# Optimization experiments

Hardware: AMD Instinct MI355X
Metric: run time of the kernel (lower is better)

Reference implementation:

```python
import jax, jax.numpy as jnp
import numpy as np

B, LQ, LK, DQ, DKEY, DV = 8, 2048, 2048, 1024, 1024, 1024
MASK_NEG = -1e6  # d2l masked_softmax fill value


def setup_inputs() -> dict:
    key = jax.random.key(0)
    kq, kk, kv, kl, kw = jax.random.split(key, 5)
    queries = jax.random.normal(kq, (B, LQ, DQ), dtype=jnp.float32)
    keys = jax.random.normal(kk, (B, LK, DKEY), dtype=jnp.float32)
    values = jax.random.normal(kv, (B, LK, DV), dtype=jnp.float32)
    valid_lens = jax.random.randint(kl, (B,), 1, LK + 1)
    W_q = jax.random.normal(kw, (DQ, DKEY), dtype=jnp.float32) / np.sqrt(DQ)
    return {"queries": queries, "keys": keys, "values": values,
            "valid_lens": valid_lens, "W_q": W_q}


def reference(queries, keys, values, valid_lens, W_q):
    # Q projection: LazyLinear(key_dim, bias=False)
    q = jnp.einsum("bqd,dk->bqk", queries, W_q)          # [B, LQ, DKEY]
    d = q.shape[-1]
    scores = jnp.einsum("bqk,bsk->bqs", q, keys) / jnp.sqrt(jnp.asarray(d, q.dtype))
    # masked_softmax: positions >= valid_len set to -1e6 before softmax
    mask = jnp.arange(scores.shape[-1])[None, None, :] < valid_lens[:, None, None]
    scores = jnp.where(mask, scores, MASK_NEG)
    attn = jax.nn.softmax(scores, axis=-1)               # [B, LQ, LK]
    # dropout p=0.0 (eval) -> identity
    return jnp.einsum("bqs,bsv->bqv", attn, values)      # [B, LQ, DV]
```

## Files before the change

kernel.cpp:

```cpp
#include <hip/hip_runtime.h>
#include <cstdint>
#include <cstddef>

#define B_   8
#define LQ_  2048
#define LK_  2048

typedef __attribute__((ext_vector_type(8))) __bf16 bf16x8;
typedef __attribute__((ext_vector_type(4))) float f32x4;
typedef __attribute__((ext_vector_type(8))) unsigned short ushortx8;

__device__ __forceinline__ unsigned short f2bf(float f) {
  unsigned u = __builtin_bit_cast(unsigned, f);
  u = u + 0x7fffu + ((u >> 16) & 1u);
  return (unsigned short)(u >> 16);
}
__device__ __forceinline__ float bf2f(unsigned short h) {
  unsigned u = ((unsigned)h) << 16;
  return __builtin_bit_cast(float, u);
}

__device__ __forceinline__ void gld_lds16(const void* g, void* l) {
  __builtin_amdgcn_global_load_lds((__attribute__((address_space(1))) void*)(void*)g,
                                   (__attribute__((address_space(3))) void*)l, 16, 0, 0);
}

__global__ __launch_bounds__(256) void cast2_bf16_kernel(
    const float* __restrict__ in0, unsigned short* __restrict__ out0,
    const float* __restrict__ in1, unsigned short* __restrict__ out1,
    size_t half_blocks) {
  const float* in = blockIdx.x < half_blocks ? in0 : in1;
  unsigned short* out = blockIdx.x < half_blocks ? out0 : out1;
  size_t bb = blockIdx.x < half_blocks ? blockIdx.x : blockIdx.x - half_blocks;
  size_t i = (bb * 256 + threadIdx.x) * 8;
  float4 a = *(const float4*)(in + i);
  float4 b = *(const float4*)(in + i + 4);
  ushortx8 o;
  o[0] = f2bf(a.x); o[1] = f2bf(a.y); o[2] = f2bf(a.z); o[3] = f2bf(a.w);
  o[4] = f2bf(b.x); o[5] = f2bf(b.y); o[6] = f2bf(b.z); o[7] = f2bf(b.w);
  *(ushortx8*)(out + i) = o;
}

__global__ __launch_bounds__(256) void transpose_cast_kernel(
    const float* __restrict__ in, unsigned short* __restrict__ out,
    int R, int C, long in_bstride, long out_bstride) {
  __shared__ float t[32][33];
  const float* inb = in + (size_t)blockIdx.z * in_bstride;
  unsigned short* outb = out + (size_t)blockIdx.z * out_bstride;
  int c0 = blockIdx.x * 32, r0 = blockIdx.y * 32;
  int tx = threadIdx.x, ty = threadIdx.y;
#pragma unroll
  for (int k = 0; k < 4; ++k) {
    int r = ty + k * 8;
    t[r][tx] = inb[(size_t)(r0 + r) * C + c0 + tx];
  }
  __syncthreads();
#pragma unroll
  for (int k = 0; k < 4; ++k) {
    int c = ty + k * 8;
    outb[(size_t)(c0 + c) * R + r0 + tx] = f2bf(t[tx][c]);
  }
}

template <int OUTM, int SKIPN, int CLAMPK>
__global__ __launch_bounds__(256) void gemm_bt_kernel(
    const unsigned short* __restrict__ A, const unsigned short* __restrict__ B,
    void* __restrict__ Cp, int M, int N, int K,
    long a_bstride, long b_bstride, long c_bstride, float scale,
    const int* __restrict__ vlp) {
  __shared__ unsigned short lA[2][128 * 64];
  __shared__ unsigned short lB[2][128 * 64];

  const int tid = threadIdx.x;
  const int wave = tid >> 6;
  const int lane = tid & 63;
  const int lane15 = lane & 15;
  const int lhalf = lane >> 4;
  const int nt = (int)((blockIdx.x + 2 * blockIdx.z) & (gridDim.x - 1));
  const int m0 = blockIdx.y * 128;
  const int n0 = nt * 128;

  int vl = K;
  if constexpr (SKIPN || CLAMPK) vl = vlp[blockIdx.z];
  if constexpr (SKIPN) {
    if (n0 >= vl) return;
  }
  int kEnd = K;
  if constexpr (CLAMPK) {
    int ke = (vl + 63) & ~63;
    kEnd = ke < K ? ke : K;
  }

  const int wm = (wave & 1) * 64;
  const int wn = (wave >> 1) * 64;

  const unsigned short* Ab = A + (size_t)blockIdx.z * a_bstride;
  const unsigned short* Bb = B + (size_t)blockIdx.z * b_bstride;

  int sr[4], sc[4], sb[4];
#pragma unroll
  for (int j = 0; j < 4; ++j) {
    int blk = (wave * 4 + j) * 64 + lane;
    sb[j] = blk;
    sr[j] = blk >> 3;
    sc[j] = ((blk & 7) ^ ((blk >> 3) & 7)) * 8;
  }

  f32x4 acc[4][4];
#pragma unroll
  for (int i = 0; i < 4; ++i)
#pragma unroll
    for (int j = 0; j < 4; ++j)
      acc[i][j] = (f32x4){0.f, 0.f, 0.f, 0.f};

  const int rswz = lane15 & 7;

#pragma unroll
  for (int j = 0; j < 4; ++j)
    gld_lds16(Ab + (size_t)(m0 + sr[j]) * K + sc[j], &lA[0][sb[j] * 8]);
#pragma unroll
  for (int j = 0; j < 4; ++j)
    gld_lds16(Bb + (size_t)(n0 + sr[j]) * K + sc[j], &lB[0][sb[j] * 8]);
  __syncthreads();

  int slot = 0;
  for (int k0 = 0; k0 < kEnd; k0 += 64) {
    if (k0 + 64 < kEnd) {
#pragma unroll
      for (int j = 0; j < 4; ++j)
        gld_lds16(Ab + (size_t)(m0 + sr[j]) * K + (k0 + 64 + sc[j]),
                  &lA[slot ^ 1][sb[j] * 8]);
#pragma unroll
      for (int j = 0; j < 4; ++j)
        gld_lds16(Bb + (size_t)(n0 + sr[j]) * K + (k0 + 64 + sc[j]),
                  &lB[slot ^ 1][sb[j] * 8]);
    }

#pragma unroll
    for (int s = 0; s < 2; ++s) {
      const int cA = ((s * 4 + lhalf) ^ rswz) * 8;
      bf16x8 af[4], bfr[4];
#pragma unroll
      for (int i = 0; i < 4; ++i)
        af[i] = *(const bf16x8*)&lA[slot][(wm + i * 16 + lane15) * 64 + cA];
#pragma unroll
      for (int j = 0; j < 4; ++j)
        bfr[j] = *(const bf16x8*)&lB[slot][(wn + j * 16 + lane15) * 64 + cA];
#pragma unroll
      for (int i = 0; i < 4; ++i)
#pragma unroll
        for (int j = 0; j < 4; ++j)
          acc[i][j] = __builtin_amdgcn_mfma_f32_16x16x32_bf16(af[i], bfr[j], acc[i][j], 0, 0, 0);
    }
    __syncthreads();
    slot ^= 1;
  }

  const size_t boffC = (size_t)blockIdx.z * c_bstride;
#pragma unroll
  for (int i = 0; i < 4; ++i) {
    int row = m0 + wm + i * 16 + lhalf * 4;
#pragma unroll
    for (int j = 0; j < 4; ++j) {
      int col = n0 + wn + j * 16 + lane15;
#pragma unroll
      for (int r = 0; r < 4; ++r) {
        float v = acc[i][j][r];
        if constexpr (OUTM == 0) {
          ((unsigned short*)Cp + boffC)[(size_t)(row + r) * N + col] = f2bf(v);
        } else if constexpr (OUTM == 1) {
          ((unsigned short*)Cp + boffC)[(size_t)(row + r) * N + col] = f2bf(v * scale);
        } else {
          ((float*)Cp + boffC)[(size_t)(row + r) * N + col] = v;
        }
      }
    }
  }
}

__global__ __launch_bounds__(256) void softmax_kernel(unsigned short* __restrict__ scores,
                                                      const int* __restrict__ valid_lens) {
  const int row = blockIdx.x;
  const int b = row >> 11;
  const int vl = valid_lens[b];
  const int kEnd = (vl + 63) & ~63;
  unsigned short* rp = scores + (size_t)row * LK_;
  const int tid = threadIdx.x;
  const int wid = tid >> 6, lane = tid & 63;
  __shared__ float sred[4];

  const int cb = tid * 8;
  const bool act = cb < kEnd;
  ushortx8 h = {};
  if (act) h = *(const ushortx8*)(rp + cb);
  float x[8];
#pragma unroll
  for (int t = 0; t < 8; ++t) x[t] = bf2f(h[t]);

  float m = -3.4e38f;
#pragma unroll
  for (int t = 0; t < 8; ++t)
    if (cb + t < vl) m = fmaxf(m, x[t]);
#pragma unroll
  for (int off = 32; off >= 1; off >>= 1) m = fmaxf(m, __shfl_xor(m, off));
  if (lane == 0) sred[wid] = m;
  __syncthreads();
  m = fmaxf(fmaxf(sred[0], sred[1]), fmaxf(sred[2], sred[3]));
  __syncthreads();

  float e[8];
  float s = 0.f;
#pragma unroll
  for (int t = 0; t < 8; ++t) {
    e[t] = (cb + t < vl) ? __expf(x[t] - m) : 0.f;
    s += e[t];
  }
#pragma unroll
  for (int off = 32; off >= 1; off >>= 1) s += __shfl_xor(s, off);
  if (lane == 0) sred[wid] = s;
  __syncthreads();
  s = sred[0] + sred[1] + sred[2] + sred[3];
  float inv = 1.f / s;

  if (act) {
    ushortx8 o;
#pragma unroll
    for (int t = 0; t < 8; ++t) o[t] = f2bf(e[t] * inv);
    *(ushortx8*)(rp + cb) = o;
  }
}

extern "C" void kernel_launch(void* const* d_in, const int* in_sizes, int n_in,
                              void* d_out, int out_size, void* d_ws, size_t ws_size,
                              hipStream_t stream) {
  const float* queries = (const float*)d_in[0];
  const float* keys = (const float*)d_in[1];
  const float* values = (const float*)d_in[2];
  const int* valid_lens = (const int*)d_in[3];
  const float* W_q = (const float*)d_in[4];
  float* out = (float*)d_out;

  unsigned short* ws = (unsigned short*)d_ws;
  const size_t M1 = (size_t)1024 * 1024;
  unsigned short* q_bf = ws;
  unsigned short* scores = ws + 16 * M1;
  unsigned short* qry_bf = scores;
  unsigned short* valsT = ws + 48 * M1;
  unsigned short* wqT = ws + 64 * M1;
  unsigned short* keys_bf = ws + 65 * M1;

  cast2_bf16_kernel<<<dim3(16384), 256, 0, stream>>>(queries, qry_bf, keys, keys_bf, 8192);
  transpose_cast_kernel<<<dim3(32, 32, 1), dim3(32, 8), 0, stream>>>(
      W_q, wqT, 1024, 1024, 0, 0);
  transpose_cast_kernel<<<dim3(32, 64, 8), dim3(32, 8), 0, stream>>>(
      values, valsT, 2048, 1024, (long)2048 * 1024, (long)1024 * 2048);
  gemm_bt_kernel<0, 0, 0><<<dim3(8, 128, 1), 256, 0, stream>>>(
      qry_bf, wqT, q_bf, 16384, 1024, 1024, 0, 0, 0, 1.f, nullptr);
  gemm_bt_kernel<1, 1, 0><<<dim3(16, 16, 8), 256, 0, stream>>>(
      q_bf, keys_bf, scores, 2048, 2048, 1024,
      (long)2048 * 1024, (long)2048 * 1024, (long)2048 * 2048, 0.03125f, valid_lens);
  softmax_kernel<<<dim3(B_ * LQ_), 256, 0, stream>>>(scores, valid_lens);
  gemm_bt_kernel<2, 0, 1><<<dim3(8, 16, 8), 256, 0, stream>>>(
      scores, valsT, out, 2048, 1024, 2048,
      (long)2048 * 2048, (long)1024 * 2048, (long)2048 * 1024, 1.f, valid_lens);
}
```

Before: 432.7 us.

## Replace 128x128 GEMM with 256x256 tile, 512-thread, 4-stage LDS pipelined kernel

All three GEMMs now use a 256x256 output tile computed by 8 waves. Each wave holds a 128x64 accumulator, and K advances in steps of 32 through a 4-deep LDS ring buffer with prefetch two stages ahead. Global-to-LDS loads are interleaved with the MFMA phases using explicit barriers, waitcnt and setprio to overlap memory and compute. The larger tile increases data reuse per block, at the cost of fewer blocks in the grid (worse load balance on valid-length-skipped tiles) and higher register pressure.

```diff
diff --git a/kernel.cpp b/kernel.cpp
--- a/kernel.cpp
+++ b/kernel.cpp
@@ -63,22 +63,22 @@
 }
 
 template <int OUTM, int SKIPN, int CLAMPK>
-__global__ __launch_bounds__(256) void gemm_bt_kernel(
+__global__ __launch_bounds__(512, 2) void gemm256_kernel(
     const unsigned short* __restrict__ A, const unsigned short* __restrict__ B,
     void* __restrict__ Cp, int M, int N, int K,
     long a_bstride, long b_bstride, long c_bstride, float scale,
     const int* __restrict__ vlp) {
-  __shared__ unsigned short lA[2][128 * 64];
-  __shared__ unsigned short lB[2][128 * 64];
+  __shared__ unsigned short lds[4][2][128 * 64];
 
   const int tid = threadIdx.x;
-  const int wave = tid >> 6;
+  const int wid = tid >> 6;
   const int lane = tid & 63;
   const int lane15 = lane & 15;
   const int lhalf = lane >> 4;
+
   const int nt = (int)((blockIdx.x + 2 * blockIdx.z) & (gridDim.x - 1));
-  const int m0 = blockIdx.y * 128;
-  const int n0 = nt * 128;
+  const int m0 = blockIdx.y * 256;
+  const int n0 = nt * 256;
 
   int vl = K;
   if constexpr (SKIPN || CLAMPK) vl = vlp[blockIdx.z];
@@ -90,82 +90,115 @@
     int ke = (vl + 63) & ~63;
     kEnd = ke < K ? ke : K;
   }
-
-  const int wm = (wave & 1) * 64;
-  const int wn = (wave >> 1) * 64;
+  const int nKt = kEnd >> 5;
 
   const unsigned short* Ab = A + (size_t)blockIdx.z * a_bstride;
   const unsigned short* Bb = B + (size_t)blockIdx.z * b_bstride;
 
-  int sr[4], sc[4], sb[4];
-#pragma unroll
-  for (int j = 0; j < 4; ++j) {
-    int blk = (wave * 4 + j) * 64 + lane;
-    sb[j] = blk;
-    sr[j] = blk >> 3;
-    sc[j] = ((blk & 7) ^ ((blk >> 3) & 7)) * 8;
-  }
-
-  f32x4 acc[4][4];
-#pragma unroll
-  for (int i = 0; i < 4; ++i)
-#pragma unroll
-    for (int j = 0; j < 4; ++j)
-      acc[i][j] = (f32x4){0.f, 0.f, 0.f, 0.f};
-
-  const int rswz = lane15 & 7;
-
-#pragma unroll
-  for (int j = 0; j < 4; ++j)
-    gld_lds16(Ab + (size_t)(m0 + sr[j]) * K + sc[j], &lA[0][sb[j] * 8]);
-#pragma unroll
-  for (int j = 0; j < 4; ++j)
-    gld_lds16(Bb + (size_t)(n0 + sr[j]) * K + sc[j], &lB[0][sb[j] * 8]);
-  __syncthreads();
-
-  int slot = 0;
-  for (int k0 = 0; k0 < kEnd; k0 += 64) {
-    if (k0 + 64 < kEnd) {
-#pragma unroll
-      for (int j = 0; j < 4; ++j)
-        gld_lds16(Ab + (size_t)(m0 + sr[j]) * K + (k0 + 64 + sc[j]),
-                  &lA[slot ^ 1][sb[j] * 8]);
-#pragma unroll
-      for (int j = 0; j < 4; ++j)
-        gld_lds16(Bb + (size_t)(n0 + sr[j]) * K + (k0 + 64 + sc[j]),
-                  &lB[slot ^ 1][sb[j] * 8]);
+  int srowA[2], srowB[2], scol[2], sdst[2];
+#pragma unroll
+  for (int j = 0; j < 2; ++j) {
+    int blk = (wid * 2 + j) * 64 + lane;
+    int p = blk >> 3, q = blk & 7;
+    int c = q ^ (p & 7);
+    int r = 2 * p + (c >> 2);
+    scol[j] = (c & 3) * 8;
+    srowA[j] = m0 + r;
+    srowB[j] = n0 + r;
+    sdst[j] = blk * 8;
+  }
+
+  const int om = (wid >> 2) * 128;
+  const int on = (wid & 3) * 64;
+  const int swz8 = ((((lane15 & 1) << 2) + lhalf) ^ ((lane15 >> 1) & 7)) << 3;
+  const int aBase = ((om >> 1) + (lane15 >> 1)) * 64 + swz8;
+  const int bBase = ((on >> 1) + (lane15 >> 1)) * 64 + swz8;
+
+  f32x4 acc[8][4];
+#pragma unroll
+  for (int f = 0; f < 8; ++f)
+#pragma unroll
+    for (int g = 0; g < 4; ++g) acc[f][g] = (f32x4){0.f, 0.f, 0.f, 0.f};
+
+#pragma unroll
+  for (int j = 0; j < 2; ++j)
+    gld_lds16(Ab + (size_t)srowA[j] * K + scol[j], &lds[0][0][sdst[j]]);
+#pragma unroll
+  for (int j = 0; j < 2; ++j)
+    gld_lds16(Bb + (size_t)srowB[j] * K + scol[j], &lds[0][1][sdst[j]]);
+#pragma unroll
+  for (int j = 0; j < 2; ++j)
+    gld_lds16(Ab + (size_t)srowA[j] * K + (32 + scol[j]), &lds[1][0][sdst[j]]);
+#pragma unroll
+  for (int j = 0; j < 2; ++j)
+    gld_lds16(Bb + (size_t)srowB[j] * K + (32 + scol[j]), &lds[1][1][sdst[j]]);
+  asm volatile("s_waitcnt vmcnt(4)" ::: "memory");
+  __builtin_amdgcn_s_barrier();
+
+  for (int t = 0; t < nKt; ++t) {
+    const unsigned short* lA = &lds[t & 3][0][0];
+    const unsigned short* lB = &lds[t & 3][1][0];
+    const bool st = (t + 2) < nKt;
+    const int nb = (t + 2) & 3;
+    const int kc = (t + 2) * 32;
+
+    bf16x8 a0[4], b0[4];
+#pragma unroll
+    for (int f = 0; f < 4; ++f) a0[f] = *(const bf16x8*)&lA[aBase + f * 512];
+#pragma unroll
+    for (int g = 0; g < 4; ++g) b0[g] = *(const bf16x8*)&lB[bBase + g * 512];
+    if (st) {
+#pragma unroll
+      for (int j = 0; j < 2; ++j)
+        gld_lds16(Ab + (size_t)srowA[j] * K + (kc + scol[j]), &lds[nb][0][sdst[j]]);
     }
-
-#pragma unroll
-    for (int s = 0; s < 2; ++s) {
-      const int cA = ((s * 4 + lhalf) ^ rswz) * 8;
-      bf16x8 af[4], bfr[4];
-#pragma unroll
-      for (int i = 0; i < 4; ++i)
-        af[i] = *(const bf16x8*)&lA[slot][(wm + i * 16 + lane15) * 64 + cA];
-#pragma unroll
-      for (int j = 0; j < 4; ++j)
-        bfr[j] = *(const bf16x8*)&lB[slot][(wn + j * 16 + lane15) * 64 + cA];
-#pragma unroll
-      for (int i = 0; i < 4; ++i)
-#pragma unroll
-        for (int j = 0; j < 4; ++j)
-          acc[i][j] = __builtin_amdgcn_mfma_f32_16x16x32_bf16(af[i], bfr[j], acc[i][j], 0, 0, 0);
+    __builtin_amdgcn_s_barrier();
+    asm volatile("s_waitcnt lgkmcnt(0)" ::: "memory");
+    __builtin_amdgcn_sched_barrier(0);
+    __builtin_amdgcn_s_setprio(1);
+#pragma unroll
+    for (int f = 0; f < 4; ++f)
+#pragma unroll
+      for (int g = 0; g < 4; ++g)
+        acc[f][g] = __builtin_amdgcn_mfma_f32_16x16x32_bf16(a0[f], b0[g], acc[f][g], 0, 0, 0);
+    __builtin_amdgcn_s_setprio(0);
+    __builtin_amdgcn_s_barrier();
+
+    bf16x8 a1[4];
+#pragma unroll
+    for (int f = 0; f < 4; ++f) a1[f] = *(const bf16x8*)&lA[aBase + (f + 4) * 512];
+    if (st) {
+#pragma unroll
+      for (int j = 0; j < 2; ++j)
+        gld_lds16(Bb + (size_t)srowB[j] * K + (kc + scol[j]), &lds[nb][1][sdst[j]]);
     }
-    __syncthreads();
-    slot ^= 1;
+    __builtin_amdgcn_s_barrier();
+    asm volatile("s_waitcnt lgkmcnt(0)" ::: "memory");
+    __builtin_amdgcn_sched_barrier(0);
+    __builtin_amdgcn_s_setprio(1);
+#pragma unroll
+    for (int f = 0; f < 4; ++f)
+#pragma unroll
+      for (int g = 0; g < 4; ++g)
+        acc[f + 4][g] = __builtin_amdgcn_mfma_f32_16x16x32_bf16(a1[f], b0[g], acc[f + 4][g], 0, 0, 0);
+    __builtin_amdgcn_s_setprio(0);
+    if (st)
+      asm volatile("s_waitcnt vmcnt(4)" ::: "memory");
+    else
+      asm volatile("s_waitcnt vmcnt(0)" ::: "memory");
+    __builtin_amdgcn_s_barrier();
   }
 
   const size_t boffC = (size_t)blockIdx.z * c_bstride;
 #pragma unroll
-  for (int i = 0; i < 4; ++i) {
-    int row = m0 + wm + i * 16 + lhalf * 4;
-#pragma unroll
-    for (int j = 0; j < 4; ++j) {
-      int col = n0 + wn + j * 16 + lane15;
+  for (int f = 0; f < 8; ++f) {
+    int row = m0 + om + f * 16 + lhalf * 4;
+#pragma unroll
+    for (int g = 0; g < 4; ++g) {
+      int col = n0 + on + g * 16 + lane15;
 #pragma unroll
       for (int r = 0; r < 4; ++r) {
-        float v = acc[i][j][r];
+        float v = acc[f][g][r];
         if constexpr (OUTM == 0) {
           ((unsigned short*)Cp + boffC)[(size_t)(row + r) * N + col] = f2bf(v);
         } else if constexpr (OUTM == 1) {
@@ -254,13 +287,13 @@
       W_q, wqT, 1024, 1024, 0, 0);
   transpose_cast_kernel<<<dim3(32, 64, 8), dim3(32, 8), 0, stream>>>(
       values, valsT, 2048, 1024, (long)2048 * 1024, (long)1024 * 2048);
-  gemm_bt_kernel<0, 0, 0><<<dim3(8, 128, 1), 256, 0, stream>>>(
+  gemm256_kernel<0, 0, 0><<<dim3(4, 64, 1), 512, 0, stream>>>(
       qry_bf, wqT, q_bf, 16384, 1024, 1024, 0, 0, 0, 1.f, nullptr);
-  gemm_bt_kernel<1, 1, 0><<<dim3(16, 16, 8), 256, 0, stream>>>(
+  gemm256_kernel<1, 1, 0><<<dim3(8, 8, 8), 512, 0, stream>>>(
       q_bf, keys_bf, scores, 2048, 2048, 1024,
       (long)2048 * 1024, (long)2048 * 1024, (long)2048 * 2048, 0.03125f, valid_lens);
   softmax_kernel<<<dim3(B_ * LQ_), 256, 0, stream>>>(scores, valid_lens);
-  gemm_bt_kernel<2, 0, 1><<<dim3(8, 16, 8), 256, 0, stream>>>(
+  gemm256_kernel<2, 0, 1><<<dim3(4, 8, 8), 512, 0, stream>>>(
       scores, valsT, out, 2048, 1024, 2048,
       (long)2048 * 2048, (long)1024 * 2048, (long)2048 * 1024, 1.f, valid_lens);
 }
```

Result: faster. 406.7 us (-6.0%).
